# Optimization experiments

Measured on AMD Instinct MI355X. Metric: run time of the kernel, lower is better.

## Reference

```python
import jax, jax.numpy as jnp
import numpy as np

N_NODES = 50000
N_EDGES = 600000
D_FT = 128   # prompt_dim == node feature dim
D_E = 32     # edge feature dim


def setup_inputs() -> dict:
    key = jax.random.key(0)
    k1, k2, k3, k4, k5 = jax.random.split(key, 5)
    graph_embedding = jax.random.normal(k1, (N_NODES, D_FT), dtype=jnp.float32)
    e_feat = jax.random.normal(k2, (N_EDGES, D_E), dtype=jnp.float32)
    weight = jax.random.normal(k3, (1, D_FT), dtype=jnp.float32)  # learned prompt
    src_idx = jax.random.randint(k4, (N_EDGES,), 0, N_NODES)
    dst_idx = jax.random.randint(k5, (N_EDGES,), 0, N_NODES)
    return {"graph_embedding": graph_embedding, "e_feat": e_feat,
            "weight": weight, "src_idx": src_idx, "dst_idx": dst_idx}


def reference(graph_embedding, e_feat, weight, src_idx, dst_idx):
    # message m = concat(src_ft * p, e); dst_ft = segment_sum(m over dst).
    # concat commutes with segment-sum, so reduce the two halves separately
    # and concatenate at node level (avoids materializing [E, D_FT+D_E]).
    src_ft = graph_embedding[src_idx] * weight            # [E, D_FT]
    agg_ft = jax.ops.segment_sum(src_ft, dst_idx, num_segments=N_NODES)
    agg_e = jax.ops.segment_sum(e_feat, dst_idx, num_segments=N_NODES)
    return jnp.concatenate([agg_ft, agg_e], axis=1)      # [N, D_FT+D_E]
```

## Files before the change

### kernel.cpp

```cpp
#include <hip/hip_runtime.h>


#define D_FT 128
#define D_E 32
#define D_OUT (D_FT + D_E)
#define CAP 32

__global__ void place_bucket_kernel(const int* __restrict__ src_idx,
                                    const int* __restrict__ dst_idx,
                                    int* __restrict__ cursor,
                                    int2* __restrict__ bucket,
                                    int* __restrict__ ovf,
                                    int* __restrict__ ovf_cnt, int E) {
    int i = blockIdx.x * blockDim.x + threadIdx.x;
    if (i >= E) return;
    int d = dst_idx[i];
    int slot = atomicAdd(&cursor[d], 1);
    if (slot < CAP) {
        int2 pr; pr.x = src_idx[i]; pr.y = i;
        bucket[(size_t)d * CAP + slot] = pr;
    } else {
        int p = atomicAdd(ovf_cnt, 1);
        ovf[p] = i;
    }
}

__global__ void gather_bucket_kernel(const float* __restrict__ emb,
                                     const float* __restrict__ e_feat,
                                     const float* __restrict__ w,
                                     const int* __restrict__ cursor,
                                     const int2* __restrict__ bucket,
                                     float* __restrict__ out, int N) {
    int g = (blockIdx.x * blockDim.x + threadIdx.x) >> 5;
    if (g >= N) return;
    int q = threadIdx.x & 31;
    int cnt = cursor[g];
    cnt = cnt > CAP ? CAP : cnt;
    int2 pr = make_int2(0, 0);
    if (q < cnt) pr = bucket[(size_t)g * CAP + q];

    float4 accft = make_float4(0.f, 0.f, 0.f, 0.f);
    float4 acce  = make_float4(0.f, 0.f, 0.f, 0.f);

    int i = 0;
    for (; i + 2 <= cnt; i += 2) {
        int s0  = __shfl(pr.x, i, 32);
        int e0  = __shfl(pr.y, i, 32);
        int s1  = __shfl(pr.x, i + 1, 32);
        int e1  = __shfl(pr.y, i + 1, 32);
        float4 v0 = *reinterpret_cast<const float4*>(emb + (size_t)s0 * D_FT + q * 4);
        float4 v1 = *reinterpret_cast<const float4*>(emb + (size_t)s1 * D_FT + q * 4);
        accft.x += v0.x + v1.x; accft.y += v0.y + v1.y;
        accft.z += v0.z + v1.z; accft.w += v0.w + v1.w;
        if (q < 8) {
            float4 a0 = *reinterpret_cast<const float4*>(e_feat + (size_t)e0 * D_E + q * 4);
            float4 a1 = *reinterpret_cast<const float4*>(e_feat + (size_t)e1 * D_E + q * 4);
            acce.x += a0.x + a1.x; acce.y += a0.y + a1.y;
            acce.z += a0.z + a1.z; acce.w += a0.w + a1.w;
        }
    }
    if (i < cnt) {
        int s0 = __shfl(pr.x, i, 32);
        int e0 = __shfl(pr.y, i, 32);
        float4 v0 = *reinterpret_cast<const float4*>(emb + (size_t)s0 * D_FT + q * 4);
        accft.x += v0.x; accft.y += v0.y; accft.z += v0.z; accft.w += v0.w;
        if (q < 8) {
            float4 a0 = *reinterpret_cast<const float4*>(e_feat + (size_t)e0 * D_E + q * 4);
            acce.x += a0.x; acce.y += a0.y; acce.z += a0.z; acce.w += a0.w;
        }
    }

    float4 wv = *reinterpret_cast<const float4*>(w + q * 4);
    float* o = out + (size_t)g * D_OUT;
    *reinterpret_cast<float4*>(o + q * 4) =
        make_float4(accft.x * wv.x, accft.y * wv.y, accft.z * wv.z, accft.w * wv.w);
    if (q < 8)
        *reinterpret_cast<float4*>(o + D_FT + q * 4) = acce;
}

__global__ void ovf_scatter_kernel(const float* __restrict__ emb,
                                   const float* __restrict__ e_feat,
                                   const float* __restrict__ w,
                                   const int* __restrict__ src_idx,
                                   const int* __restrict__ dst_idx,
                                   const int* __restrict__ ovf,
                                   const int* __restrict__ ovf_cnt,
                                   float* __restrict__ out) {
    int n = *ovf_cnt;
    int total = n * 40;
    for (int t = blockIdx.x * blockDim.x + threadIdx.x; t < total;
         t += gridDim.x * blockDim.x) {
        int e = t / 40, slot = t % 40;
        int eid = ovf[e];
        int d = dst_idx[eid];
        float* o = out + (size_t)d * D_OUT;
        if (slot < 32) {
            int s = src_idx[eid];
            float4 v  = *reinterpret_cast<const float4*>(emb + (size_t)s * D_FT + slot * 4);
            float4 wv = *reinterpret_cast<const float4*>(w + slot * 4);
            atomicAdd(o + slot * 4 + 0, v.x * wv.x);
            atomicAdd(o + slot * 4 + 1, v.y * wv.y);
            atomicAdd(o + slot * 4 + 2, v.z * wv.z);
            atomicAdd(o + slot * 4 + 3, v.w * wv.w);
        } else {
            int q = slot - 32;
            float4 ve = *reinterpret_cast<const float4*>(e_feat + (size_t)eid * D_E + q * 4);
            atomicAdd(o + D_FT + q * 4 + 0, ve.x);
            atomicAdd(o + D_FT + q * 4 + 1, ve.y);
            atomicAdd(o + D_FT + q * 4 + 2, ve.z);
            atomicAdd(o + D_FT + q * 4 + 3, ve.w);
        }
    }
}

__global__ void scatter_ft_kernel(const float* __restrict__ emb, const float* __restrict__ w,
                                  const int* __restrict__ src_idx, const int* __restrict__ dst_idx,
                                  float* __restrict__ out, int n_items) {
    int idx = blockIdx.x * blockDim.x + threadIdx.x;
    if (idx >= n_items) return;
    int e = idx >> 5, q = idx & 31;
    int s = src_idx[e], d = dst_idx[e];
    const float4 v  = *reinterpret_cast<const float4*>(emb + (size_t)s * D_FT + q * 4);
    const float4 wv = *reinterpret_cast<const float4*>(w + q * 4);
    float* o = out + (size_t)d * D_OUT + q * 4;
    atomicAdd(o + 0, v.x * wv.x); atomicAdd(o + 1, v.y * wv.y);
    atomicAdd(o + 2, v.z * wv.z); atomicAdd(o + 3, v.w * wv.w);
}
__global__ void scatter_e_kernel(const float* __restrict__ e_feat, const int* __restrict__ dst_idx,
                                 float* __restrict__ out, int n_items) {
    int idx = blockIdx.x * blockDim.x + threadIdx.x;
    if (idx >= n_items) return;
    int e = idx >> 3, q = idx & 7;
    int d = dst_idx[e];
    const float4 v = *reinterpret_cast<const float4*>(e_feat + (size_t)e * D_E + q * 4);
    float* o = out + (size_t)d * D_OUT + D_FT + q * 4;
    atomicAdd(o + 0, v.x); atomicAdd(o + 1, v.y);
    atomicAdd(o + 2, v.z); atomicAdd(o + 3, v.w);
}

extern "C" void kernel_launch(void* const* d_in, const int* in_sizes, int n_in,
                              void* d_out, int out_size, void* d_ws, size_t ws_size,
                              hipStream_t stream) {
    const float* emb    = (const float*)d_in[0];
    const float* e_feat = (const float*)d_in[1];
    const float* w      = (const float*)d_in[2];
    const int*   src    = (const int*)d_in[3];
    const int*   dst    = (const int*)d_in[4];
    float* out = (float*)d_out;

    const int E = in_sizes[3];
    const int N = out_size / D_OUT;

    size_t ints_head = (size_t)N + 2;
    size_t need = ints_head * 4 + (size_t)N * CAP * 8 + (size_t)E * 4;

    if (ws_size >= need) {
        int*  cursor  = (int*)d_ws;
        int*  ovf_cnt = cursor + N;
        int2* bucket  = (int2*)(cursor + ints_head);
        int*  ovf     = (int*)(bucket + (size_t)N * CAP);

        hipMemsetAsync(cursor, 0, ints_head * sizeof(int), stream);
        place_bucket_kernel<<<(E + 255) / 256, 256, 0, stream>>>(
            src, dst, cursor, bucket, ovf, ovf_cnt, E);
        gather_bucket_kernel<<<((size_t)N * 32 + 255) / 256, 256, 0, stream>>>(
            emb, e_feat, w, cursor, bucket, out, N);
        ovf_scatter_kernel<<<256, 256, 0, stream>>>(
            emb, e_feat, w, src, dst, ovf, ovf_cnt, out);
    } else {
        hipMemsetAsync(d_out, 0, (size_t)out_size * sizeof(float), stream);
        int items_ft = E * 32, items_e = E * 8;
        scatter_ft_kernel<<<(items_ft + 255) / 256, 256, 0, stream>>>(emb, w, src, dst, out, items_ft);
        scatter_e_kernel<<<(items_e + 255) / 256, 256, 0, stream>>>(e_feat, dst, out, items_e);
    }
}
```

Before: 102.8 us.

## Gather two nodes per warp with 4-wide masked loads and fold overflow handling

The gather kernel now processes two destination nodes per 32-lane group and unrolls by four with clamped, masked loads. This raises memory-level parallelism and avoids divergent tails. Edge-feature loads are spread across all 32 lanes (four edges per iteration) and combined with xor shuffles. The separate atomic overflow kernel is removed; groups whose node overflowed now scan the overflow list themselves, which saves a launch but is serial per group if overflow is large. Nontemporal loads and stores are added for bucket, edge features and output.

```diff
diff --git a/kernel.cpp b/kernel.cpp
--- a/kernel.cpp
+++ b/kernel.cpp
@@ -6,10 +6,18 @@
 #define D_OUT (D_FT + D_E)
 #define CAP 32
 
+typedef float f32x4 __attribute__((ext_vector_type(4)));
+typedef int   i32x2 __attribute__((ext_vector_type(2)));
+
+__device__ __forceinline__ int clampi(int t, int hi) {
+    t = t > hi ? hi : t;
+    return t < 0 ? 0 : t;
+}
+
 __global__ void place_bucket_kernel(const int* __restrict__ src_idx,
                                     const int* __restrict__ dst_idx,
                                     int* __restrict__ cursor,
-                                    int2* __restrict__ bucket,
+                                    i32x2* __restrict__ bucket,
                                     int* __restrict__ ovf,
                                     int* __restrict__ ovf_cnt, int E) {
     int i = blockIdx.x * blockDim.x + threadIdx.x;
@@ -17,8 +25,8 @@
     int d = dst_idx[i];
     int slot = atomicAdd(&cursor[d], 1);
     if (slot < CAP) {
-        int2 pr; pr.x = src_idx[i]; pr.y = i;
-        bucket[(size_t)d * CAP + slot] = pr;
+        i32x2 pr; pr.x = src_idx[i]; pr.y = i;
+        __builtin_nontemporal_store(pr, &bucket[(size_t)d * CAP + slot]);
     } else {
         int p = atomicAdd(ovf_cnt, 1);
         ovf[p] = i;
@@ -29,86 +37,146 @@
                                      const float* __restrict__ e_feat,
                                      const float* __restrict__ w,
                                      const int* __restrict__ cursor,
-                                     const int2* __restrict__ bucket,
+                                     const i32x2* __restrict__ bucket,
+                                     const int* __restrict__ src_idx,
+                                     const int* __restrict__ dst_idx,
+                                     const int* __restrict__ ovf,
+                                     const int* __restrict__ ovf_cnt,
                                      float* __restrict__ out, int N) {
-    int g = (blockIdx.x * blockDim.x + threadIdx.x) >> 5;
-    if (g >= N) return;
-    int q = threadIdx.x & 31;
-    int cnt = cursor[g];
-    cnt = cnt > CAP ? CAP : cnt;
-    int2 pr = make_int2(0, 0);
-    if (q < cnt) pr = bucket[(size_t)g * CAP + q];
-
-    float4 accft = make_float4(0.f, 0.f, 0.f, 0.f);
-    float4 acce  = make_float4(0.f, 0.f, 0.f, 0.f);
-
-    int i = 0;
-    for (; i + 2 <= cnt; i += 2) {
-        int s0  = __shfl(pr.x, i, 32);
-        int e0  = __shfl(pr.y, i, 32);
-        int s1  = __shfl(pr.x, i + 1, 32);
-        int e1  = __shfl(pr.y, i + 1, 32);
-        float4 v0 = *reinterpret_cast<const float4*>(emb + (size_t)s0 * D_FT + q * 4);
-        float4 v1 = *reinterpret_cast<const float4*>(emb + (size_t)s1 * D_FT + q * 4);
-        accft.x += v0.x + v1.x; accft.y += v0.y + v1.y;
-        accft.z += v0.z + v1.z; accft.w += v0.w + v1.w;
+    int grp = (blockIdx.x * blockDim.x + threadIdx.x) >> 5;
+    int ga = grp * 2;
+    if (ga >= N) return;
+    int gb = ga + 1;
+    const int q  = threadIdx.x & 31;
+    const int qg = q >> 3;
+    const int ql = q & 7;
+
+    int2 cc = *reinterpret_cast<const int2*>(cursor + ga);
+    int rawa = cc.x;
+    int rawb = (gb < N) ? cc.y : 0;
+    int cnta = rawa > CAP ? CAP : rawa;
+    int cntb = rawb > CAP ? CAP : rawb;
+
+    i32x2 pra; pra.x = 0; pra.y = 0;
+    i32x2 prb; prb.x = 0; prb.y = 0;
+    if (q < cnta) pra = __builtin_nontemporal_load(&bucket[(size_t)ga * CAP + q]);
+    if (q < cntb) prb = __builtin_nontemporal_load(&bucket[(size_t)gb * CAP + q]);
+
+    float4 fa = make_float4(0.f, 0.f, 0.f, 0.f);
+    float4 fb = make_float4(0.f, 0.f, 0.f, 0.f);
+    float4 ea = make_float4(0.f, 0.f, 0.f, 0.f);
+    float4 eb = make_float4(0.f, 0.f, 0.f, 0.f);
+
+    const int ca = cnta - 1, cb = cntb - 1;
+    const int mx = cnta > cntb ? cnta : cntb;
+    for (int i = 0; i < mx; i += 4) {
+        int sa0 = __shfl(pra.x, clampi(i + 0, ca), 32);
+        int sa1 = __shfl(pra.x, clampi(i + 1, ca), 32);
+        int sa2 = __shfl(pra.x, clampi(i + 2, ca), 32);
+        int sa3 = __shfl(pra.x, clampi(i + 3, ca), 32);
+        int sb0 = __shfl(prb.x, clampi(i + 0, cb), 32);
+        int sb1 = __shfl(prb.x, clampi(i + 1, cb), 32);
+        int sb2 = __shfl(prb.x, clampi(i + 2, cb), 32);
+        int sb3 = __shfl(prb.x, clampi(i + 3, cb), 32);
+        int eia = __shfl(pra.y, clampi(i + qg, ca), 32);
+        int eib = __shfl(prb.y, clampi(i + qg, cb), 32);
+
+        float4 va0 = *reinterpret_cast<const float4*>(emb + (size_t)sa0 * D_FT + q * 4);
+        float4 va1 = *reinterpret_cast<const float4*>(emb + (size_t)sa1 * D_FT + q * 4);
+        float4 va2 = *reinterpret_cast<const float4*>(emb + (size_t)sa2 * D_FT + q * 4);
+        float4 va3 = *reinterpret_cast<const float4*>(emb + (size_t)sa3 * D_FT + q * 4);
+        float4 vb0 = *reinterpret_cast<const float4*>(emb + (size_t)sb0 * D_FT + q * 4);
+        float4 vb1 = *reinterpret_cast<const float4*>(emb + (size_t)sb1 * D_FT + q * 4);
+        float4 vb2 = *reinterpret_cast<const float4*>(emb + (size_t)sb2 * D_FT + q * 4);
+        float4 vb3 = *reinterpret_cast<const float4*>(emb + (size_t)sb3 * D_FT + q * 4);
+        f32x4 aea = __builtin_nontemporal_load(
+            reinterpret_cast<const f32x4*>(e_feat + (size_t)eia * D_E + ql * 4));
+        f32x4 aeb = __builtin_nontemporal_load(
+            reinterpret_cast<const f32x4*>(e_feat + (size_t)eib * D_E + ql * 4));
+
+        float ma0 = (i + 0 < cnta) ? 1.f : 0.f;
+        float ma1 = (i + 1 < cnta) ? 1.f : 0.f;
+        float ma2 = (i + 2 < cnta) ? 1.f : 0.f;
+        float ma3 = (i + 3 < cnta) ? 1.f : 0.f;
+        float mb0 = (i + 0 < cntb) ? 1.f : 0.f;
+        float mb1 = (i + 1 < cntb) ? 1.f : 0.f;
+        float mb2 = (i + 2 < cntb) ? 1.f : 0.f;
+        float mb3 = (i + 3 < cntb) ? 1.f : 0.f;
+        float mea = (i + qg < cnta) ? 1.f : 0.f;
+        float meb = (i + qg < cntb) ? 1.f : 0.f;
+
+        fa.x = fmaf(va0.x, ma0, fa.x); fa.y = fmaf(va0.y, ma0, fa.y);
+        fa.z = fmaf(va0.z, ma0, fa.z); fa.w = fmaf(va0.w, ma0, fa.w);
+        fa.x = fmaf(va1.x, ma1, fa.x); fa.y = fmaf(va1.y, ma1, fa.y);
+        fa.z = fmaf(va1.z, ma1, fa.z); fa.w = fmaf(va1.w, ma1, fa.w);
+        fa.x = fmaf(va2.x, ma2, fa.x); fa.y = fmaf(va2.y, ma2, fa.y);
+        fa.z = fmaf(va2.z, ma2, fa.z); fa.w = fmaf(va2.w, ma2, fa.w);
+        fa.x = fmaf(va3.x, ma3, fa.x); fa.y = fmaf(va3.y, ma3, fa.y);
+        fa.z = fmaf(va3.z, ma3, fa.z); fa.w = fmaf(va3.w, ma3, fa.w);
+        fb.x = fmaf(vb0.x, mb0, fb.x); fb.y = fmaf(vb0.y, mb0, fb.y);
+        fb.z = fmaf(vb0.z, mb0, fb.z); fb.w = fmaf(vb0.w, mb0, fb.w);
+        fb.x = fmaf(vb1.x, mb1, fb.x); fb.y = fmaf(vb1.y, mb1, fb.y);
+        fb.z = fmaf(vb1.z, mb1, fb.z); fb.w = fmaf(vb1.w, mb1, fb.w);
+        fb.x = fmaf(vb2.x, mb2, fb.x); fb.y = fmaf(vb2.y, mb2, fb.y);
+        fb.z = fmaf(vb2.z, mb2, fb.z); fb.w = fmaf(vb2.w, mb2, fb.w);
+        fb.x = fmaf(vb3.x, mb3, fb.x); fb.y = fmaf(vb3.y, mb3, fb.y);
+        fb.z = fmaf(vb3.z, mb3, fb.z); fb.w = fmaf(vb3.w, mb3, fb.w);
+        ea.x = fmaf(aea.x, mea, ea.x); ea.y = fmaf(aea.y, mea, ea.y);
+        ea.z = fmaf(aea.z, mea, ea.z); ea.w = fmaf(aea.w, mea, ea.w);
+        eb.x = fmaf(aeb.x, meb, eb.x); eb.y = fmaf(aeb.y, meb, eb.y);
+        eb.z = fmaf(aeb.z, meb, eb.z); eb.w = fmaf(aeb.w, meb, eb.w);
+    }
+
+    if (rawa > CAP || rawb > CAP) {
+        int n = *ovf_cnt;
+        for (int k = 0; k < n; ++k) {
+            int eid = ovf[k];
+            int dd = dst_idx[eid];
+            bool isa = (dd == ga), isb = (dd == gb);
+            if (isa || isb) {
+                int s = src_idx[eid];
+                float4 v = *reinterpret_cast<const float4*>(emb + (size_t)s * D_FT + q * 4);
+                f32x4 af = __builtin_nontemporal_load(
+                    reinterpret_cast<const f32x4*>(e_feat + (size_t)eid * D_E + ql * 4));
+                if (isa) {
+                    fa.x += v.x; fa.y += v.y; fa.z += v.z; fa.w += v.w;
+                    if (q < 8) { ea.x += af.x; ea.y += af.y; ea.z += af.z; ea.w += af.w; }
+                } else {
+                    fb.x += v.x; fb.y += v.y; fb.z += v.z; fb.w += v.w;
+                    if (q < 8) { eb.x += af.x; eb.y += af.y; eb.z += af.z; eb.w += af.w; }
+                }
+            }
+        }
+    }
+
+    ea.x += __shfl_xor(ea.x, 8, 32);  ea.y += __shfl_xor(ea.y, 8, 32);
+    ea.z += __shfl_xor(ea.z, 8, 32);  ea.w += __shfl_xor(ea.w, 8, 32);
+    ea.x += __shfl_xor(ea.x, 16, 32); ea.y += __shfl_xor(ea.y, 16, 32);
+    ea.z += __shfl_xor(ea.z, 16, 32); ea.w += __shfl_xor(ea.w, 16, 32);
+    eb.x += __shfl_xor(eb.x, 8, 32);  eb.y += __shfl_xor(eb.y, 8, 32);
+    eb.z += __shfl_xor(eb.z, 8, 32);  eb.w += __shfl_xor(eb.w, 8, 32);
+    eb.x += __shfl_xor(eb.x, 16, 32); eb.y += __shfl_xor(eb.y, 16, 32);
+    eb.z += __shfl_xor(eb.z, 16, 32); eb.w += __shfl_xor(eb.w, 16, 32);
+
+    float4 wv = *reinterpret_cast<const float4*>(w + q * 4);
+    {
+        float* oa = out + (size_t)ga * D_OUT;
+        f32x4 r; r.x = fa.x * wv.x; r.y = fa.y * wv.y;
+                 r.z = fa.z * wv.z; r.w = fa.w * wv.w;
+        __builtin_nontemporal_store(r, reinterpret_cast<f32x4*>(oa + q * 4));
         if (q < 8) {
-            float4 a0 = *reinterpret_cast<const float4*>(e_feat + (size_t)e0 * D_E + q * 4);
-            float4 a1 = *reinterpret_cast<const float4*>(e_feat + (size_t)e1 * D_E + q * 4);
-            acce.x += a0.x + a1.x; acce.y += a0.y + a1.y;
-            acce.z += a0.z + a1.z; acce.w += a0.w + a1.w;
+            f32x4 re; re.x = ea.x; re.y = ea.y; re.z = ea.z; re.w = ea.w;
+            __builtin_nontemporal_store(re, reinterpret_cast<f32x4*>(oa + D_FT + q * 4));
         }
     }
-    if (i < cnt) {
-        int s0 = __shfl(pr.x, i, 32);
-        int e0 = __shfl(pr.y, i, 32);
-        float4 v0 = *reinterpret_cast<const float4*>(emb + (size_t)s0 * D_FT + q * 4);
-        accft.x += v0.x; accft.y += v0.y; accft.z += v0.z; accft.w += v0.w;
+    if (gb < N) {
+        float* ob = out + (size_t)gb * D_OUT;
+        f32x4 r; r.x = fb.x * wv.x; r.y = fb.y * wv.y;
+                 r.z = fb.z * wv.z; r.w = fb.w * wv.w;
+        __builtin_nontemporal_store(r, reinterpret_cast<f32x4*>(ob + q * 4));
         if (q < 8) {
-            float4 a0 = *reinterpret_cast<const float4*>(e_feat + (size_t)e0 * D_E + q * 4);
-            acce.x += a0.x; acce.y += a0.y; acce.z += a0.z; acce.w += a0.w;
-        }
-    }
-
-    float4 wv = *reinterpret_cast<const float4*>(w + q * 4);
-    float* o = out + (size_t)g * D_OUT;
-    *reinterpret_cast<float4*>(o + q * 4) =
-        make_float4(accft.x * wv.x, accft.y * wv.y, accft.z * wv.z, accft.w * wv.w);
-    if (q < 8)
-        *reinterpret_cast<float4*>(o + D_FT + q * 4) = acce;
-}
-
-__global__ void ovf_scatter_kernel(const float* __restrict__ emb,
-                                   const float* __restrict__ e_feat,
-                                   const float* __restrict__ w,
-                                   const int* __restrict__ src_idx,
-                                   const int* __restrict__ dst_idx,
-                                   const int* __restrict__ ovf,
-                                   const int* __restrict__ ovf_cnt,
-                                   float* __restrict__ out) {
-    int n = *ovf_cnt;
-    int total = n * 40;
-    for (int t = blockIdx.x * blockDim.x + threadIdx.x; t < total;
-         t += gridDim.x * blockDim.x) {
-        int e = t / 40, slot = t % 40;
-        int eid = ovf[e];
-        int d = dst_idx[eid];
-        float* o = out + (size_t)d * D_OUT;
-        if (slot < 32) {
-            int s = src_idx[eid];
-            float4 v  = *reinterpret_cast<const float4*>(emb + (size_t)s * D_FT + slot * 4);
-            float4 wv = *reinterpret_cast<const float4*>(w + slot * 4);
-            atomicAdd(o + slot * 4 + 0, v.x * wv.x);
-            atomicAdd(o + slot * 4 + 1, v.y * wv.y);
-            atomicAdd(o + slot * 4 + 2, v.z * wv.z);
-            atomicAdd(o + slot * 4 + 3, v.w * wv.w);
-        } else {
-            int q = slot - 32;
-            float4 ve = *reinterpret_cast<const float4*>(e_feat + (size_t)eid * D_E + q * 4);
-            atomicAdd(o + D_FT + q * 4 + 0, ve.x);
-            atomicAdd(o + D_FT + q * 4 + 1, ve.y);
-            atomicAdd(o + D_FT + q * 4 + 2, ve.z);
-            atomicAdd(o + D_FT + q * 4 + 3, ve.w);
+            f32x4 re; re.x = eb.x; re.y = eb.y; re.z = eb.z; re.w = eb.w;
+            __builtin_nontemporal_store(re, reinterpret_cast<f32x4*>(ob + D_FT + q * 4));
         }
     }
 }
@@ -155,18 +223,17 @@
     size_t need = ints_head * 4 + (size_t)N * CAP * 8 + (size_t)E * 4;
 
     if (ws_size >= need) {
-        int*  cursor  = (int*)d_ws;
-        int*  ovf_cnt = cursor + N;
-        int2* bucket  = (int2*)(cursor + ints_head);
-        int*  ovf     = (int*)(bucket + (size_t)N * CAP);
+        int*   cursor  = (int*)d_ws;
+        int*   ovf_cnt = cursor + N;
+        i32x2* bucket  = (i32x2*)(cursor + ints_head);
+        int*   ovf     = (int*)(bucket + (size_t)N * CAP);
 
         hipMemsetAsync(cursor, 0, ints_head * sizeof(int), stream);
         place_bucket_kernel<<<(E + 255) / 256, 256, 0, stream>>>(
             src, dst, cursor, bucket, ovf, ovf_cnt, E);
-        gather_bucket_kernel<<<((size_t)N * 32 + 255) / 256, 256, 0, stream>>>(
-            emb, e_feat, w, cursor, bucket, out, N);
-        ovf_scatter_kernel<<<256, 256, 0, stream>>>(
-            emb, e_feat, w, src, dst, ovf, ovf_cnt, out);
+        int groups = (N + 1) / 2;
+        gather_bucket_kernel<<<((size_t)groups * 32 + 255) / 256, 256, 0, stream>>>(
+            emb, e_feat, w, cursor, bucket, src, dst, ovf, ovf_cnt, out, N);
     } else {
         hipMemsetAsync(d_out, 0, (size_t)out_size * sizeof(float), stream);
         int items_ft = E * 32, items_e = E * 8;
```

New measurement: 113.5 us. +10.4%, slower.
